# Optimization experiments

Hardware: AMD Instinct MI355X
Metric: run time of the kernel (lower is better)

Reference implementation:

```python
import math
import jax, jax.numpy as jnp
import numpy as np

D_MODEL = 768
N_HEADS = 12


def setup_inputs() -> dict:
    key = jax.random.key(0)
    kx, kw, kb = jax.random.split(key, 3)
    x = jax.random.normal(kx, (2, 2048, D_MODEL), dtype=jnp.float32)
    # nn.Linear(D, 3D): weight [3D, D], bias [3D]; init ~ U(-1/sqrt(D), 1/sqrt(D))
    bound = 1.0 / math.sqrt(D_MODEL)
    W_kqv = jax.random.uniform(kw, (3 * D_MODEL, D_MODEL), dtype=jnp.float32, minval=-bound, maxval=bound)
    b_kqv = jax.random.uniform(kb, (3 * D_MODEL,), dtype=jnp.float32, minval=-bound, maxval=bound)
    return {"x": x, "W_kqv": W_kqv, "b_kqv": b_kqv}


def reference(x, W_kqv, b_kqv):
    N, C, D = x.shape
    H = N_HEADS
    hd = D // H
    z = jnp.einsum('ncd,ed->nce', x, W_kqv) + b_kqv  # [N, C, 3D]
    # order in source: k first, then q, then v
    k = z[:, :, :D].reshape(N, C, H, hd).transpose(0, 2, 1, 3)       # [N,H,C,hd]
    q = z[:, :, D:2 * D].reshape(N, C, H, hd).transpose(0, 2, 1, 3)
    v = z[:, :, 2 * D:].reshape(N, C, H, hd).transpose(0, 2, 1, 3)
    # NOTE: faithful to source: scale by sqrt(D) (full model dim), not sqrt(head_dim)
    scores = jnp.einsum('nhqd,nhkd->nhqk', q, k) / math.sqrt(D)
    causal = jnp.tril(jnp.ones((C, C), dtype=bool))
    scores = jnp.where(causal, scores, -jnp.inf)
    attn = jax.nn.softmax(scores, axis=-1)
    out = jnp.einsum('nhqk,nhkd->nhqd', attn, v)  # [N,H,C,hd]
    return out.transpose(0, 2, 1, 3).reshape(N, C, D)
```

## Files before the change

### kernel.cpp

```cpp
#include <hip/hip_runtime.h>
#include <stdint.h>

#define D_MODEL 768
#define E3      2304
#define NCTX    2048
#define NH      12
#define HD      64
#define MROWS   4096
#define NHTOT   24

typedef __attribute__((ext_vector_type(8))) short short8;
typedef __attribute__((ext_vector_type(4))) short bf16x4;
typedef __attribute__((ext_vector_type(4))) float f32x4;

typedef __attribute__((address_space(3))) uint32_t lds_u32;
typedef __attribute__((address_space(1))) uint32_t glob_u32;

__device__ __forceinline__ void async_copy16(const void* g, void* l) {
    __builtin_amdgcn_global_load_lds((const glob_u32*)(uintptr_t)g,
                                     (lds_u32*)(uint32_t)(uintptr_t)l, 16, 0, 0);
}

__device__ __forceinline__ unsigned short f2bf(float f) {
    uint32_t u = __builtin_bit_cast(uint32_t, f);
    u += 0x7fffu + ((u >> 16) & 1u);
    return (unsigned short)(u >> 16);
}

__device__ __forceinline__ float fast_exp2(float x) {
#if __has_builtin(__builtin_amdgcn_exp2f)
    return __builtin_amdgcn_exp2f(x);
#else
    return __expf(x * 0.6931471805599453f);
#endif
}

#if __has_builtin(__builtin_amdgcn_mfma_f32_16x16x16bf16_1k)
#define HAVE_MFMA16 1
#else
#define HAVE_MFMA16 0
#endif

__global__ __launch_bounds__(256) void cast2_bf16_kernel(const float* __restrict__ a,
                                                         unsigned short* __restrict__ oa,
                                                         int na4,
                                                         const float* __restrict__ b,
                                                         unsigned short* __restrict__ ob) {
    int i = blockIdx.x * blockDim.x + threadIdx.x;
    const float4* src;
    ushort4* dst;
    int idx;
    if (i < na4) { src = (const float4*)a; dst = (ushort4*)oa; idx = i; }
    else         { src = (const float4*)b; dst = (ushort4*)ob; idx = i - na4; }
    float4 v = src[idx];
    ushort4 o;
    o.x = f2bf(v.x); o.y = f2bf(v.y); o.z = f2bf(v.z); o.w = f2bf(v.w);
    dst[idx] = o;
}

__global__ __launch_bounds__(256) void qkv_gemm(const unsigned short* __restrict__ A,
                                                const unsigned short* __restrict__ B,
                                                const float* __restrict__ bias,
                                                unsigned short* __restrict__ Zq,
                                                unsigned short* __restrict__ Kb,
                                                unsigned short* __restrict__ Vb) {
    __shared__ __attribute__((aligned(16))) unsigned short sA[128 * 64];
    __shared__ __attribute__((aligned(16))) unsigned short sB[128 * 64];

    const int tid  = threadIdx.x;
    const int wave = tid >> 6;
    const int lane = tid & 63;
    const int quad = lane >> 4;
    const int l15  = lane & 15;
    const int wm   = (wave >> 1) << 6;
    const int wn   = (wave & 1) << 6;
    const int row0 = blockIdx.y * 128;
    const int col0 = blockIdx.x * 128;

    const int srow   = lane >> 3;
    const int schunk = (lane & 7) * 8;

    f32x4 acc[4][4] = {};

    for (int k0 = 0; k0 < D_MODEL; k0 += 64) {
        __syncthreads();
#pragma unroll
        for (int c = 0; c < 4; ++c) {
            const int rbase = wave * 32 + c * 8;
            async_copy16(A + (size_t)(row0 + rbase + srow) * D_MODEL + k0 + schunk, &sA[rbase * 64]);
            async_copy16(B + (size_t)(col0 + rbase + srow) * D_MODEL + k0 + schunk, &sB[rbase * 64]);
        }
        __syncthreads();

#pragma unroll
        for (int ks = 0; ks < 2; ++ks) {
            short8 aF[4], bF[4];
#pragma unroll
            for (int i = 0; i < 4; ++i)
                aF[i] = *(const short8*)&sA[(wm + i * 16 + l15) * 64 + ks * 32 + quad * 8];
#pragma unroll
            for (int i = 0; i < 4; ++i)
                bF[i] = *(const short8*)&sB[(wn + i * 16 + l15) * 64 + ks * 32 + quad * 8];
#pragma unroll
            for (int i = 0; i < 4; ++i)
#pragma unroll
                for (int j = 0; j < 4; ++j)
                    acc[i][j] = __builtin_amdgcn_mfma_f32_16x16x32_bf16(aF[i], bF[j], acc[i][j], 0, 0, 0);
        }
    }

    if (col0 < D_MODEL) {
#pragma unroll
        for (int j = 0; j < 4; ++j) {
            const int col = col0 + wn + j * 16 + l15;
            const float bv = bias[col];
            const int h = col >> 6, d = col & 63;
            const int ks = d >> 5, quadd = (d >> 3) & 3, e = d & 7;
#pragma unroll
            for (int i = 0; i < 4; ++i) {
                const int row = row0 + wm + i * 16 + quad * 4;
                const int n = row >> 11;
                const int key = row & (NCTX - 1);
                const int kb = key >> 6;
                const int ct = i;
                const size_t base = ((size_t)((n * NH + h) * 32 + kb)) * 4096
                                  + (((ks * 4 + ct) * 4 + quadd) * 16) * 8 + e;
#pragma unroll
                for (int r = 0; r < 4; ++r)
                    Kb[base + (size_t)(quad * 4 + r) * 8] = f2bf(acc[i][j][r] + bv);
            }
        }
    } else if (col0 < 2 * D_MODEL) {
        const float zscale = 0.036084391824351615f * 1.4426950408889634f;
#pragma unroll
        for (int j = 0; j < 4; ++j) {
            const int col = col0 - D_MODEL + wn + j * 16 + l15;
            const float bv = bias[col0 + wn + j * 16 + l15];
#pragma unroll
            for (int i = 0; i < 4; ++i) {
                const int row = row0 + wm + i * 16 + quad * 4;
#pragma unroll
                for (int r = 0; r < 4; ++r)
                    Zq[(size_t)(row + r) * D_MODEL + col] = f2bf((acc[i][j][r] + bv) * zscale);
            }
        }
    } else {
#pragma unroll
        for (int j = 0; j < 4; ++j) {
            const int col = col0 + wn + j * 16 + l15;
            const float bv = bias[col];
            const int ch = col - 2 * D_MODEL;
            const int h = ch >> 6, d = ch & 63;
            const int dt = d >> 4, l15d = d & 15;
#pragma unroll
            for (int i = 0; i < 4; ++i) {
                const int row = row0 + wm + i * 16 + quad * 4;
                const int n = row >> 11;
                const int key = row & (NCTX - 1);
                const int kb = key >> 6;
                const int ct = i, quadv = quad;
                ushort4 w4;
                w4.x = f2bf(acc[i][j][0] + bv);
                w4.y = f2bf(acc[i][j][1] + bv);
                w4.z = f2bf(acc[i][j][2] + bv);
                w4.w = f2bf(acc[i][j][3] + bv);
                *(ushort4*)&Vb[((size_t)((n * NH + h) * 32 + kb)) * 4096
                               + (((ct * 4 + dt) * 4 + quadv) * 16 + l15d) * 4] = w4;
            }
        }
    }
}

__global__ __launch_bounds__(256) void attn_kernel(const unsigned short* __restrict__ Zq,
                                                   const unsigned short* __restrict__ Kb,
                                                   const unsigned short* __restrict__ Vb,
                                                   float* __restrict__ out) {
    __shared__ __attribute__((aligned(16))) unsigned short sK[3][4096];
    __shared__ __attribute__((aligned(16))) unsigned short sV[3][4096];
#if !HAVE_MFMA16
    __shared__ __attribute__((aligned(16))) unsigned short sP[4][16 * 72];
#endif

    const int tid  = threadIdx.x;
    const int wave = tid >> 6;
    const int lane = tid & 63;
    const int quad = lane >> 4;
    const int l15  = lane & 15;
    const int b    = blockIdx.x;
    const int xcd  = b & 7;
    const int ii   = b >> 3;
    const int t    = 31 - ii / 3;
    const int nh   = (ii % 3) * 8 + xcd;
    const int n    = nh / NH;
    const int h    = nh - n * NH;

    const unsigned short* KbP = Kb + (size_t)(nh * 32) * 4096;
    const unsigned short* VbP = Vb + (size_t)(nh * 32) * 4096;

    const unsigned short* Qp = Zq + (size_t)(n * NCTX + t * 64 + wave * 16) * D_MODEL + h * HD;
    short8 qf[2];
#pragma unroll
    for (int ks = 0; ks < 2; ++ks)
        qf[ks] = *(const short8*)&Qp[(size_t)l15 * D_MODEL + ks * 32 + quad * 8];

    f32x4 o[4] = {};
    float lsum = 0.0f;

#define STAGE(kbi, bufi)                                                          \
    do {                                                                          \
        const size_t gof = (size_t)(kbi) * 4096;                                  \
        _Pragma("unroll")                                                         \
        for (int c = 0; c < 2; ++c) {                                             \
            const int off = wave * 1024 + c * 512;                                \
            async_copy16(KbP + gof + off + lane * 8, &sK[bufi][off]);             \
            async_copy16(VbP + gof + off + lane * 8, &sV[bufi][off]);             \
        }                                                                         \
    } while (0)

    STAGE(0, 0);
    if (t >= 1) STAGE(1, 1);

    int cb = 0;
    for (int kb = 0; kb <= t; ++kb) {
        if (kb == t) { asm volatile("s_waitcnt vmcnt(0)" ::: "memory"); }
        else         { asm volatile("s_waitcnt vmcnt(4)" ::: "memory"); }
        __builtin_amdgcn_s_barrier();
        __builtin_amdgcn_sched_barrier(0);

        if (kb + 2 <= t) {
            int nb = cb + 2; if (nb >= 3) nb -= 3;
            STAGE(kb + 2, nb);
        }

        short8 kf[2][4];
#pragma unroll
        for (int ks = 0; ks < 2; ++ks)
#pragma unroll
            for (int ct = 0; ct < 4; ++ct)
                kf[ks][ct] = *(const short8*)&sK[cb][(ks * 4 + ct) * 512 + lane * 8];

        f32x4 s[4] = {};
        __builtin_amdgcn_s_setprio(1);
#pragma unroll
        for (int ct = 0; ct < 4; ++ct) {
            s[ct] = __builtin_amdgcn_mfma_f32_16x16x32_bf16(kf[0][ct], qf[0], s[ct], 0, 0, 0);
            s[ct] = __builtin_amdgcn_mfma_f32_16x16x32_bf16(kf[1][ct], qf[1], s[ct], 0, 0, 0);
        }
        __builtin_amdgcn_s_setprio(0);

        const bool diag = (kb == t);
        const int qg = t * 64 + wave * 16 + l15;
#if HAVE_MFMA16
        bf16x4 pA[4];
#endif
#pragma unroll
        for (int ct = 0; ct < 4; ++ct) {
            float pv[4];
#pragma unroll
            for (int r = 0; r < 4; ++r) {
                const int key = kb * 64 + ct * 16 + quad * 4 + r;
                float sv = s[ct][r];
                if (diag && key > qg) sv = -INFINITY;
                pv[r] = fast_exp2(sv);
                lsum += pv[r];
            }
#if HAVE_MFMA16
            pA[ct][0] = (short)f2bf(pv[0]); pA[ct][1] = (short)f2bf(pv[1]);
            pA[ct][2] = (short)f2bf(pv[2]); pA[ct][3] = (short)f2bf(pv[3]);
#else
            ushort4 w4;
            w4.x = f2bf(pv[0]); w4.y = f2bf(pv[1]); w4.z = f2bf(pv[2]); w4.w = f2bf(pv[3]);
            *(ushort4*)&sP[wave][l15 * 72 + ct * 16 + quad * 4] = w4;
#endif
        }

#if HAVE_MFMA16
        __builtin_amdgcn_s_setprio(1);
#pragma unroll
        for (int ct = 0; ct < 4; ++ct)
#pragma unroll
            for (int dt = 0; dt < 4; ++dt) {
                const bf16x4 vf = *(const bf16x4*)&sV[cb][(ct * 4 + dt) * 256 + lane * 4];
                o[dt] = __builtin_amdgcn_mfma_f32_16x16x16bf16_1k(pA[ct], vf, o[dt], 0, 0, 0);
            }
        __builtin_amdgcn_s_setprio(0);
#else
        const short8 pf0 = *(const short8*)&sP[wave][l15 * 72 + quad * 8];
        const short8 pf1 = *(const short8*)&sP[wave][l15 * 72 + 32 + quad * 8];
#pragma unroll
        for (int dt = 0; dt < 4; ++dt) {
            short8 vf0, vf1;
#pragma unroll
            for (int e = 0; e < 8; ++e) {
                const int k0 = quad * 8 + e;
                const int k1 = 32 + quad * 8 + e;
                vf0[e] = (short)sV[cb][(((k0 >> 4) * 4 + dt) * 4 + ((k0 >> 2) & 3)) * 64 + l15 * 4 + (k0 & 3)];
                vf1[e] = (short)sV[cb][(((k1 >> 4) * 4 + dt) * 4 + ((k1 >> 2) & 3)) * 64 + l15 * 4 + (k1 & 3)];
            }
            o[dt] = __builtin_amdgcn_mfma_f32_16x16x32_bf16(pf0, vf0, o[dt], 0, 0, 0);
            o[dt] = __builtin_amdgcn_mfma_f32_16x16x32_bf16(pf1, vf1, o[dt], 0, 0, 0);
        }
#endif
        cb = (cb + 1 == 3) ? 0 : cb + 1;
    }
#undef STAGE

    float l = lsum;
    l += __shfl_xor(l, 16);
    l += __shfl_xor(l, 32);
    const float linv = 1.0f / l;
#pragma unroll
    for (int r = 0; r < 4; ++r) {
        const float inv = __shfl(linv, quad * 4 + r);
        const size_t row = (size_t)n * NCTX + t * 64 + wave * 16 + quad * 4 + r;
#pragma unroll
        for (int dt = 0; dt < 4; ++dt)
            out[row * D_MODEL + h * HD + dt * 16 + l15] = o[dt][r] * inv;
    }
}

extern "C" void kernel_launch(void* const* d_in, const int* in_sizes, int n_in,
                              void* d_out, int out_size, void* d_ws, size_t ws_size,
                              hipStream_t stream) {
    const float* x = (const float*)d_in[0];
    const float* W = (const float*)d_in[1];
    const float* b = (const float*)d_in[2];
    float* out = (float*)d_out;

    unsigned short* xb = (unsigned short*)d_ws;
    unsigned short* Wb = xb + (size_t)MROWS * D_MODEL;
    unsigned short* Zq = Wb + (size_t)E3 * D_MODEL;
    unsigned short* Kb = Zq + (size_t)MROWS * D_MODEL;
    unsigned short* Vb = Kb + (size_t)NHTOT * 32 * 4096;

    const int NA4 = MROWS * D_MODEL / 4;
    const int NW4 = E3 * D_MODEL / 4;
    cast2_bf16_kernel<<<dim3((NA4 + NW4) / 256), 256, 0, stream>>>(x, xb, NA4, W, Wb);
    qkv_gemm<<<dim3(E3 / 128, MROWS / 128), 256, 0, stream>>>(xb, Wb, b, Zq, Kb, Vb);
    attn_kernel<<<dim3(NHTOT * (NCTX / 64)), 256, 0, stream>>>(Zq, Kb, Vb, out);
}
```

Measured before the change: 153.1 us.

## Split attention key range across two wave groups per block with LDS reduction

Doubles the attention block to 512 threads; each half of the waves processes half of the causal key blocks for the same 64 query rows, each half with its own double-buffered K/V tiles. Partial outputs and row sums from the second half are reduced through LDS before the final normalise and store. This shortens the serial key loop for long causal rows and adds intra-block parallelism, at the cost of a full-block barrier each iteration, dropping from triple to double buffering, removing the setprio hints, and an extra reduction step.

```diff
diff --git a/kernel.cpp b/kernel.cpp
--- a/kernel.cpp
+++ b/kernel.cpp
@@ -171,18 +171,20 @@
     }
 }
 
-__global__ __launch_bounds__(256) void attn_kernel(const unsigned short* __restrict__ Zq,
+__global__ __launch_bounds__(512) void attn_kernel(const unsigned short* __restrict__ Zq,
                                                    const unsigned short* __restrict__ Kb,
                                                    const unsigned short* __restrict__ Vb,
                                                    float* __restrict__ out) {
-    __shared__ __attribute__((aligned(16))) unsigned short sK[3][4096];
-    __shared__ __attribute__((aligned(16))) unsigned short sV[3][4096];
+    __shared__ __attribute__((aligned(16))) unsigned short sK[2][2][4096];
+    __shared__ __attribute__((aligned(16))) unsigned short sV[2][2][4096];
 #if !HAVE_MFMA16
-    __shared__ __attribute__((aligned(16))) unsigned short sP[4][16 * 72];
+    __shared__ __attribute__((aligned(16))) unsigned short sP[8][16 * 72];
 #endif
 
     const int tid  = threadIdx.x;
     const int wave = tid >> 6;
+    const int half = wave >> 2;
+    const int wv   = wave & 3;
     const int lane = tid & 63;
     const int quad = lane >> 4;
     const int l15  = lane & 15;
@@ -194,10 +196,15 @@
     const int n    = nh / NH;
     const int h    = nh - n * NH;
 
+    const int nA    = (t + 2) >> 1;
+    const int nB    = t + 1 - nA;
+    const int kbase = half ? nA : 0;
+    const int nMy   = half ? nB : nA;
+
     const unsigned short* KbP = Kb + (size_t)(nh * 32) * 4096;
     const unsigned short* VbP = Vb + (size_t)(nh * 32) * 4096;
 
-    const unsigned short* Qp = Zq + (size_t)(n * NCTX + t * 64 + wave * 16) * D_MODEL + h * HD;
+    const unsigned short* Qp = Zq + (size_t)(n * NCTX + t * 64 + wv * 16) * D_MODEL + h * HD;
     short8 qf[2];
 #pragma unroll
     for (int ks = 0; ks < 2; ++ks)
@@ -211,111 +218,120 @@
         const size_t gof = (size_t)(kbi) * 4096;                                  \
         _Pragma("unroll")                                                         \
         for (int c = 0; c < 2; ++c) {                                             \
-            const int off = wave * 1024 + c * 512;                                \
-            async_copy16(KbP + gof + off + lane * 8, &sK[bufi][off]);             \
-            async_copy16(VbP + gof + off + lane * 8, &sV[bufi][off]);             \
+            const int off = wv * 1024 + c * 512;                                  \
+            async_copy16(KbP + gof + off + lane * 8, &sK[half][bufi][off]);       \
+            async_copy16(VbP + gof + off + lane * 8, &sV[half][bufi][off]);       \
         }                                                                         \
     } while (0)
 
-    STAGE(0, 0);
-    if (t >= 1) STAGE(1, 1);
-
-    int cb = 0;
-    for (int kb = 0; kb <= t; ++kb) {
-        if (kb == t) { asm volatile("s_waitcnt vmcnt(0)" ::: "memory"); }
-        else         { asm volatile("s_waitcnt vmcnt(4)" ::: "memory"); }
-        __builtin_amdgcn_s_barrier();
-        __builtin_amdgcn_sched_barrier(0);
-
-        if (kb + 2 <= t) {
-            int nb = cb + 2; if (nb >= 3) nb -= 3;
-            STAGE(kb + 2, nb);
-        }
-
-        short8 kf[2][4];
-#pragma unroll
-        for (int ks = 0; ks < 2; ++ks)
+    if (nMy > 0) STAGE(kbase, 0);
+
+    for (int i = 0; i < nA; ++i) {
+        __syncthreads();
+        if (i + 1 < nMy) STAGE(kbase + i + 1, (i + 1) & 1);
+
+        if (i < nMy) {
+            const int kb  = kbase + i;
+            const int buf = i & 1;
+
+            short8 kf[2][4];
+#pragma unroll
+            for (int ks = 0; ks < 2; ++ks)
+#pragma unroll
+                for (int ct = 0; ct < 4; ++ct)
+                    kf[ks][ct] = *(const short8*)&sK[half][buf][(ks * 4 + ct) * 512 + lane * 8];
+
+            f32x4 s[4] = {};
+#pragma unroll
+            for (int ct = 0; ct < 4; ++ct) {
+                s[ct] = __builtin_amdgcn_mfma_f32_16x16x32_bf16(kf[0][ct], qf[0], s[ct], 0, 0, 0);
+                s[ct] = __builtin_amdgcn_mfma_f32_16x16x32_bf16(kf[1][ct], qf[1], s[ct], 0, 0, 0);
+            }
+
+            const bool diag = (kb == t);
+            const int qg = t * 64 + wv * 16 + l15;
+#if HAVE_MFMA16
+            bf16x4 pA[4];
+#endif
+#pragma unroll
+            for (int ct = 0; ct < 4; ++ct) {
+                float pv[4];
+#pragma unroll
+                for (int r = 0; r < 4; ++r) {
+                    const int key = kb * 64 + ct * 16 + quad * 4 + r;
+                    float sv = s[ct][r];
+                    if (diag && key > qg) sv = -INFINITY;
+                    pv[r] = fast_exp2(sv);
+                    lsum += pv[r];
+                }
+#if HAVE_MFMA16
+                pA[ct][0] = (short)f2bf(pv[0]); pA[ct][1] = (short)f2bf(pv[1]);
+                pA[ct][2] = (short)f2bf(pv[2]); pA[ct][3] = (short)f2bf(pv[3]);
+#else
+                ushort4 w4;
+                w4.x = f2bf(pv[0]); w4.y = f2bf(pv[1]); w4.z = f2bf(pv[2]); w4.w = f2bf(pv[3]);
+                *(ushort4*)&sP[wave][l15 * 72 + ct * 16 + quad * 4] = w4;
+#endif
+            }
+
+#if HAVE_MFMA16
 #pragma unroll
             for (int ct = 0; ct < 4; ++ct)
-                kf[ks][ct] = *(const short8*)&sK[cb][(ks * 4 + ct) * 512 + lane * 8];
-
-        f32x4 s[4] = {};
-        __builtin_amdgcn_s_setprio(1);
-#pragma unroll
-        for (int ct = 0; ct < 4; ++ct) {
-            s[ct] = __builtin_amdgcn_mfma_f32_16x16x32_bf16(kf[0][ct], qf[0], s[ct], 0, 0, 0);
-            s[ct] = __builtin_amdgcn_mfma_f32_16x16x32_bf16(kf[1][ct], qf[1], s[ct], 0, 0, 0);
-        }
-        __builtin_amdgcn_s_setprio(0);
-
-        const bool diag = (kb == t);
-        const int qg = t * 64 + wave * 16 + l15;
-#if HAVE_MFMA16
-        bf16x4 pA[4];
-#endif
-#pragma unroll
-        for (int ct = 0; ct < 4; ++ct) {
-            float pv[4];
-#pragma unroll
-            for (int r = 0; r < 4; ++r) {
-                const int key = kb * 64 + ct * 16 + quad * 4 + r;
-                float sv = s[ct][r];
-                if (diag && key > qg) sv = -INFINITY;
-                pv[r] = fast_exp2(sv);
-                lsum += pv[r];
-            }
-#if HAVE_MFMA16
-            pA[ct][0] = (short)f2bf(pv[0]); pA[ct][1] = (short)f2bf(pv[1]);
-            pA[ct][2] = (short)f2bf(pv[2]); pA[ct][3] = (short)f2bf(pv[3]);
+#pragma unroll
+                for (int dt = 0; dt < 4; ++dt) {
+                    const bf16x4 vf = *(const bf16x4*)&sV[half][buf][(ct * 4 + dt) * 256 + lane * 4];
+                    o[dt] = __builtin_amdgcn_mfma_f32_16x16x16bf16_1k(pA[ct], vf, o[dt], 0, 0, 0);
+                }
 #else
-            ushort4 w4;
-            w4.x = f2bf(pv[0]); w4.y = f2bf(pv[1]); w4.z = f2bf(pv[2]); w4.w = f2bf(pv[3]);
-            *(ushort4*)&sP[wave][l15 * 72 + ct * 16 + quad * 4] = w4;
-#endif
-        }
-
-#if HAVE_MFMA16
-        __builtin_amdgcn_s_setprio(1);
-#pragma unroll
-        for (int ct = 0; ct < 4; ++ct)
+            const short8 pf0 = *(const short8*)&sP[wave][l15 * 72 + quad * 8];
+            const short8 pf1 = *(const short8*)&sP[wave][l15 * 72 + 32 + quad * 8];
 #pragma unroll
             for (int dt = 0; dt < 4; ++dt) {
-                const bf16x4 vf = *(const bf16x4*)&sV[cb][(ct * 4 + dt) * 256 + lane * 4];
-                o[dt] = __builtin_amdgcn_mfma_f32_16x16x16bf16_1k(pA[ct], vf, o[dt], 0, 0, 0);
-            }
-        __builtin_amdgcn_s_setprio(0);
-#else
-        const short8 pf0 = *(const short8*)&sP[wave][l15 * 72 + quad * 8];
-        const short8 pf1 = *(const short8*)&sP[wave][l15 * 72 + 32 + quad * 8];
-#pragma unroll
-        for (int dt = 0; dt < 4; ++dt) {
-            short8 vf0, vf1;
-#pragma unroll
-            for (int e = 0; e < 8; ++e) {
-                const int k0 = quad * 8 + e;
-                const int k1 = 32 + quad * 8 + e;
-                vf0[e] = (short)sV[cb][(((k0 >> 4) * 4 + dt) * 4 + ((k0 >> 2) & 3)) * 64 + l15 * 4 + (k0 & 3)];
-                vf1[e] = (short)sV[cb][(((k1 >> 4) * 4 + dt) * 4 + ((k1 >> 2) & 3)) * 64 + l15 * 4 + (k1 & 3)];
-            }
-            o[dt] = __builtin_amdgcn_mfma_f32_16x16x32_bf16(pf0, vf0, o[dt], 0, 0, 0);
-            o[dt] = __builtin_amdgcn_mfma_f32_16x16x32_bf16(pf1, vf1, o[dt], 0, 0, 0);
-        }
-#endif
-        cb = (cb + 1 == 3) ? 0 : cb + 1;
+                short8 vf0, vf1;
+#pragma unroll
+                for (int e = 0; e < 8; ++e) {
+                    const int k0 = quad * 8 + e;
+                    const int k1 = 32 + quad * 8 + e;
+                    vf0[e] = (short)sV[half][buf][(((k0 >> 4) * 4 + dt) * 4 + ((k0 >> 2) & 3)) * 64 + l15 * 4 + (k0 & 3)];
+                    vf1[e] = (short)sV[half][buf][(((k1 >> 4) * 4 + dt) * 4 + ((k1 >> 2) & 3)) * 64 + l15 * 4 + (k1 & 3)];
+                }
+                o[dt] = __builtin_amdgcn_mfma_f32_16x16x32_bf16(pf0, vf0, o[dt], 0, 0, 0);
+                o[dt] = __builtin_amdgcn_mfma_f32_16x16x32_bf16(pf1, vf1, o[dt], 0, 0, 0);
+            }
+#endif
+        }
     }
 #undef STAGE
 
     float l = lsum;
     l += __shfl_xor(l, 16);
     l += __shfl_xor(l, 32);
-    const float linv = 1.0f / l;
-#pragma unroll
-    for (int r = 0; r < 4; ++r) {
-        const float inv = __shfl(linv, quad * 4 + r);
-        const size_t row = (size_t)n * NCTX + t * 64 + wave * 16 + quad * 4 + r;
+
+    __syncthreads();
+    float* red = (float*)&sK[0][0][0];
+    if (half == 1) {
+        float* po = red + wv * 1040;
 #pragma unroll
         for (int dt = 0; dt < 4; ++dt)
-            out[row * D_MODEL + h * HD + dt * 16 + l15] = o[dt][r] * inv;
+#pragma unroll
+            for (int r = 0; r < 4; ++r)
+                po[(quad * 4 + r) * 64 + dt * 16 + l15] = o[dt][r];
+        if (quad == 0) po[1024 + l15] = l;
+    }
+    __syncthreads();
+    if (half == 0) {
+        const float* po = red + wv * 1040;
+        const float l2 = po[1024 + l15];
+        const float linv = 1.0f / (l + l2);
+#pragma unroll
+        for (int r = 0; r < 4; ++r) {
+            const float inv = __shfl(linv, quad * 4 + r);
+            const size_t row = (size_t)n * NCTX + t * 64 + wv * 16 + quad * 4 + r;
+#pragma unroll
+            for (int dt = 0; dt < 4; ++dt)
+                out[row * D_MODEL + h * HD + dt * 16 + l15] =
+                    (o[dt][r] + po[(quad * 4 + r) * 64 + dt * 16 + l15]) * inv;
+        }
     }
 }
 
@@ -337,5 +353,5 @@
     const int NW4 = E3 * D_MODEL / 4;
     cast2_bf16_kernel<<<dim3((NA4 + NW4) / 256), 256, 0, stream>>>(x, xb, NA4, W, Wb);
     qkv_gemm<<<dim3(E3 / 128, MROWS / 128), 256, 0, stream>>>(xb, Wb, b, Zq, Kb, Vb);
-    attn_kernel<<<dim3(NHTOT * (NCTX / 64)), 256, 0, stream>>>(Zq, Kb, Vb, out);
-}
+    attn_kernel<<<dim3(NHTOT * (NCTX / 64)), 512, 0, stream>>>(Zq, Kb, Vb, out);
+}
```

New measurement: 140.5 us. 8.2% less time.
